# Optimization experiments

Measured on AMD Instinct MI355X. Metric: run time of the kernel, lower is better.

Reference implementation:

```python
import jax, jax.numpy as jnp
import numpy as np

B, I, H, L = 1048576, 14, 16, 8  # batch, input_size, hidden_size, num_layers


def setup_inputs() -> dict:
    key = jax.random.key(0)
    ks = jax.random.split(key, 9)
    s = 1.0 / np.sqrt(H)  # torch LSTM init scale
    return {
        "x": jax.random.normal(ks[0], (B, I), dtype=jnp.float32),
        "W_ih0": jax.random.uniform(ks[1], (4 * H, I), minval=-s, maxval=s),
        "W_ih": jax.random.uniform(ks[2], (L - 1, 4 * H, H), minval=-s, maxval=s),
        "W_hh": jax.random.uniform(ks[3], (L, 4 * H, H), minval=-s, maxval=s),
        "b_ih": jax.random.uniform(ks[4], (L, 4 * H), minval=-s, maxval=s),
        "b_hh": jax.random.uniform(ks[5], (L, 4 * H), minval=-s, maxval=s),
        "fc_w": jax.random.uniform(ks[6], (1, H), minval=-s, maxval=s),
        "fc_b": jax.random.uniform(ks[7], (1,), minval=-s, maxval=s),
    }


def _cell(inp, h, c, Wi, Wh, bi, bh):
    # PyTorch gate order: i, f, g, o
    g = inp @ Wi.T + bi + h @ Wh.T + bh  # [B, 4H]
    i, f, gg, o = jnp.split(g, 4, axis=-1)
    c_new = jax.nn.sigmoid(f) * c + jax.nn.sigmoid(i) * jnp.tanh(gg)
    h_new = jax.nn.sigmoid(o) * jnp.tanh(c_new)
    return h_new, c_new


def reference(x, W_ih0, W_ih, W_hh, b_ih, b_hh, fc_w, fc_b):
    # seq_len == 1, so each nn.LSTM layer is one cell step.
    # Original quirk: for layers >= 1 the layer input AND initial hidden are
    # both the previous layer's output h; initial cell is previous layer's c.
    h = jnp.zeros((x.shape[0], H), x.dtype)
    c = jnp.zeros_like(h)
    h, c = _cell(x, h, c, W_ih0, W_hh[0], b_ih[0], b_hh[0])
    for l in range(1, L):  # fixed small layer count
        h, c = _cell(h, h, c, W_ih[l - 1], W_hh[l], b_ih[l], b_hh[l])
    return h @ fc_w.T + fc_b  # [B, 1]
```

## Files before the change

### kernel.cpp

```cpp
#include <hip/hip_runtime.h>


typedef _Float16 f16x8 __attribute__((ext_vector_type(8)));
typedef _Float16 f16x2 __attribute__((ext_vector_type(2)));
typedef float f32x4 __attribute__((ext_vector_type(4)));
typedef float f32x2 __attribute__((ext_vector_type(2)));

#if __has_builtin(__builtin_amdgcn_mfma_f32_16x16x32_f16)
__device__ __forceinline__ f32x4 mfma32h(f16x8 a, f16x8 b, f32x4 c) {
    return __builtin_amdgcn_mfma_f32_16x16x32_f16(a, b, c, 0, 0, 0);
}
#else
__device__ __forceinline__ f32x4 mfma32h(f16x8 a, f16x8 b, f32x4 c) {
    asm volatile("v_mfma_f32_16x16x32_f16 %0, %1, %2, %0\n\ts_nop 7\n\ts_nop 7"
                 : "+v"(c) : "v"(a), "v"(b));
    return c;
}
#endif

#define NLOG2E  (-1.4426950408889634f)
#define G2LOG2E (2.8853900817779268f)
#define THREADS 1024
#define WAVES_PB (THREADS / 64)
#define NBLOCKS 512
#define NTILES 3

__device__ __forceinline__ void act2(f32x2 yi, f32x2 yf, f32x2 yg, f32x2 yo,
                                     f32x2& c, f32x2& h) {
    f32x2 Ei, Ef, Eg, Eo;
    Ei[0] = __builtin_amdgcn_exp2f(yi[0]); Ei[1] = __builtin_amdgcn_exp2f(yi[1]);
    Ef[0] = __builtin_amdgcn_exp2f(yf[0]); Ef[1] = __builtin_amdgcn_exp2f(yf[1]);
    Eg[0] = __builtin_amdgcn_exp2f(yg[0]); Eg[1] = __builtin_amdgcn_exp2f(yg[1]);
    Eo[0] = __builtin_amdgcn_exp2f(yo[0]); Eo[1] = __builtin_amdgcn_exp2f(yo[1]);
    const f32x2 one = {1.f, 1.f};
    const f32x2 Di = Ei + one, Df = Ef + one, Do = Eo + one;
    const f32x2 P = __builtin_elementwise_fma(Di, Eg, Di);
    const f32x2 num = __builtin_elementwise_fma(
        Eg, Df, __builtin_elementwise_fma(c, P, -Df));
    const f32x2 DfP = Df * P;
    f32x2 R1;
    R1[0] = __builtin_amdgcn_rcpf(DfP[0]); R1[1] = __builtin_amdgcn_rcpf(DfP[1]);
    c = num * R1;
    const f32x2 cg = c * (f32x2){G2LOG2E, G2LOG2E};
    f32x2 Ec;
    Ec[0] = __builtin_amdgcn_exp2f(cg[0]); Ec[1] = __builtin_amdgcn_exp2f(cg[1]);
    const f32x2 Q = __builtin_elementwise_fma(Do, Ec, Do);
    f32x2 R2;
    R2[0] = __builtin_amdgcn_rcpf(Q[0]); R2[1] = __builtin_amdgcn_rcpf(Q[1]);
    h = __builtin_elementwise_fma(Ec, R2, -R2);
}

#define LOP(v) __builtin_shufflevector(v, v, 0, 1)
#define HIP2(v) __builtin_shufflevector(v, v, 2, 3)

__device__ __forceinline__ f16x8 make_bfrag(f32x2 ha, f32x2 hb) {
    const f16x2 p0 = __builtin_bit_cast(f16x2, __builtin_amdgcn_cvt_pkrtz(ha[0], ha[1]));
    const f16x2 p1 = __builtin_bit_cast(f16x2, __builtin_amdgcn_cvt_pkrtz(hb[0], hb[1]));
    return (f16x8){p0[0], p0[1], p1[0], p1[1], p0[0], p0[1], p1[0], p1[1]};
}

__global__ __launch_bounds__(THREADS, 2) void lstm_mfma_kernel(
    const float* __restrict__ x,
    const float* __restrict__ W_ih0,
    const float* __restrict__ W_ih,
    const float* __restrict__ W_hh,
    const float* __restrict__ b_ih,
    const float* __restrict__ b_hh,
    const float* __restrict__ fc_w,
    const float* __restrict__ fc_b,
    float* __restrict__ out,
    int nB)
{
    __shared__ __align__(16) short sWF[8 * 4 * 64 * 8];
    __shared__ __align__(16) float sB[8 * 64];
    __shared__ __align__(16) float sFC[20];

    const int tid = threadIdx.x;

    for (int slot = tid; slot < 2048; slot += THREADS) {
        const int l = slot >> 8;
        const int t = (slot >> 6) & 3;
        const int ln = slot & 63;
        const int row = t * 16 + (ln & 15);
        const int k0 = (ln >> 4) * 4;
        const float scale = (t == 2) ? G2LOG2E : NLOG2E;
        short frag[8];
        #pragma unroll
        for (int j = 0; j < 4; ++j) {
            const int k = k0 + j;
            float w;
            if (l == 0) w = (k < 14) ? W_ih0[row * 14 + k] : 0.0f;
            else        w = W_ih[(l - 1) * 1024 + row * 16 + k]
                          + W_hh[l * 1024 + row * 16 + k];
            w *= scale;
            const _Float16 wh = (_Float16)w;
            const float wres = w - (float)wh;
            const _Float16 wl = (_Float16)wres;
            frag[j]     = __builtin_bit_cast(short, wh);
            frag[4 + j] = __builtin_bit_cast(short, wl);
        }
        *(short4*)(sWF + slot * 8)     = make_short4(frag[0], frag[1], frag[2], frag[3]);
        *(short4*)(sWF + slot * 8 + 4) = make_short4(frag[4], frag[5], frag[6], frag[7]);
    }
    for (int idx = tid; idx < 512; idx += THREADS) {
        const int row = idx & 63;
        const float scale = ((row >> 4) == 2) ? G2LOG2E : NLOG2E;
        sB[idx] = (b_ih[idx] + b_hh[idx]) * scale;
    }
    if (tid < 16) sFC[tid] = fc_w[tid];
    if (tid == 16) sFC[16] = fc_b[0];
    __syncthreads();

    const int lane = tid & 63;
    const int wv = tid >> 6;
    const int bcol = lane & 15;
    const int hi = lane >> 4;

    const int n_grp = (nB + (16 * NTILES - 1)) / (16 * NTILES);
    const int waves_total = NBLOCKS * WAVES_PB;
    const int iters = (n_grp + waves_total - 1) / waves_total;
    const int gw = blockIdx.x * WAVES_PB + wv;

    const short* wbase = sWF + (lane << 3);
    const float* bbase = sB + hi * 4;

    const f32x4 fw4 = *(const f32x4*)(sFC + hi * 4);
    const f32x2 fwa = LOP(fw4), fwb = HIP2(fw4);
    const float fb = sFC[16];

    for (int it = 0; it < iters; ++it) {
        const int grp = gw * iters + it;
        if (grp >= n_grp) break;

        int bidx[NTILES];
        f32x2 ha[NTILES], hb[NTILES];
        f16x8 Bf[NTILES];
        f32x2 ca[NTILES], cb[NTILES];

        #pragma unroll
        for (int m = 0; m < NTILES; ++m) {
            const int b = grp * (16 * NTILES) + m * 16 + bcol;
            bidx[m] = b;
            const int bc = b < nB ? b : nB - 1;
            const float* xr = x + bc * 14 + hi * 4;
            const float2 p = *(const float2*)xr;
            ha[m][0] = p.x; ha[m][1] = p.y;
            if (hi < 3) {
                const float2 q = *(const float2*)(xr + 2);
                hb[m][0] = q.x; hb[m][1] = q.y;
            } else { hb[m] = (f32x2){0.f, 0.f}; }
            Bf[m] = make_bfrag(ha[m], hb[m]);
            ca[m] = (f32x2){0.f, 0.f};
            cb[m] = (f32x2){0.f, 0.f};
        }

        #pragma unroll
        for (int l = 0; l < 8; ++l) {
            f16x8 fr[4];
            f32x4 bias[4];
            #pragma unroll
            for (int t = 0; t < 4; ++t) {
                fr[t] = *(const f16x8*)(wbase + ((l * 4 + t) << 9));
                bias[t] = *(const f32x4*)(bbase + l * 64 + t * 16);
            }
            #pragma unroll
            for (int m = 0; m < NTILES; ++m) {
                f32x4 a[4];
                #pragma unroll
                for (int t = 0; t < 4; ++t) {
                    a[t] = mfma32h(fr[t], Bf[m], bias[t]);
                }
                act2(LOP(a[0]), LOP(a[1]), LOP(a[2]), LOP(a[3]), ca[m], ha[m]);
                act2(HIP2(a[0]), HIP2(a[1]), HIP2(a[2]), HIP2(a[3]), cb[m], hb[m]);
                Bf[m] = make_bfrag(ha[m], hb[m]);
            }
        }

        #pragma unroll
        for (int m = 0; m < NTILES; ++m) {
            f32x2 s = ha[m] * fwa;
            s = __builtin_elementwise_fma(hb[m], fwb, s);
            float p = s[0] + s[1];
            p += __shfl_xor(p, 16, 64);
            p += __shfl_xor(p, 32, 64);
            if (hi == 0 && bidx[m] < nB) out[bidx[m]] = p + fb;
        }
    }
}

extern "C" void kernel_launch(void* const* d_in, const int* in_sizes, int n_in,
                              void* d_out, int out_size, void* d_ws, size_t ws_size,
                              hipStream_t stream) {
    const float* x     = (const float*)d_in[0];
    const float* W_ih0 = (const float*)d_in[1];
    const float* W_ih  = (const float*)d_in[2];
    const float* W_hh  = (const float*)d_in[3];
    const float* b_ih  = (const float*)d_in[4];
    const float* b_hh  = (const float*)d_in[5];
    const float* fc_w  = (const float*)d_in[6];
    const float* fc_b  = (const float*)d_in[7];
    float* out = (float*)d_out;

    const int B = in_sizes[0] / 14;
    lstm_mfma_kernel<<<NBLOCKS, THREADS, 0, stream>>>(
        x, W_ih0, W_ih, W_hh, b_ih, b_hh, fc_w, fc_b, out, B);
}
```

Measured before the change: 124.5 us.

## Prefetch next batch group's inputs and interleave two tiles' MFMAs per layer

```diff
diff --git a/kernel.cpp b/kernel.cpp
--- a/kernel.cpp
+++ b/kernel.cpp
@@ -23,7 +23,7 @@
 #define THREADS 1024
 #define WAVES_PB (THREADS / 64)
 #define NBLOCKS 512
-#define NTILES 3
+#define NTILES 2
 
 __device__ __forceinline__ void act2(f32x2 yi, f32x2 yf, f32x2 yg, f32x2 yo,
                                      f32x2& c, f32x2& h) {
@@ -59,7 +59,7 @@
     return (f16x8){p0[0], p0[1], p1[0], p1[1], p0[0], p0[1], p1[0], p1[1]};
 }
 
-__global__ __launch_bounds__(THREADS, 2) void lstm_mfma_kernel(
+__global__ __launch_bounds__(THREADS, 8) void lstm_mfma_kernel(
     const float* __restrict__ x,
     const float* __restrict__ W_ih0,
     const float* __restrict__ W_ih,
@@ -120,6 +120,7 @@
     const int waves_total = NBLOCKS * WAVES_PB;
     const int iters = (n_grp + waves_total - 1) / waves_total;
     const int gw = blockIdx.x * WAVES_PB + wv;
+    const int grp_base = gw * iters;
 
     const short* wbase = sWF + (lane << 3);
     const float* bbase = sB + hi * 4;
@@ -128,52 +129,57 @@
     const f32x2 fwa = LOP(fw4), fwb = HIP2(fw4);
     const float fb = sFC[16];
 
+    int pf_b[NTILES];
+    float2 pf_a[NTILES], pf_q[NTILES];
+    auto prefetch = [&](int grp) {
+        #pragma unroll
+        for (int m = 0; m < NTILES; ++m) {
+            const int b = grp * (16 * NTILES) + m * 16 + bcol;
+            pf_b[m] = b;
+            const int bc = b < nB ? b : nB - 1;
+            const float* xr = x + bc * 14 + hi * 4;
+            pf_a[m] = *(const float2*)xr;
+            pf_q[m] = (hi < 3) ? *(const float2*)(xr + 2) : make_float2(0.f, 0.f);
+        }
+    };
+
+    if (grp_base < n_grp) prefetch(grp_base);
+
     for (int it = 0; it < iters; ++it) {
-        const int grp = gw * iters + it;
+        const int grp = grp_base + it;
         if (grp >= n_grp) break;
 
         int bidx[NTILES];
         f32x2 ha[NTILES], hb[NTILES];
         f16x8 Bf[NTILES];
         f32x2 ca[NTILES], cb[NTILES];
-
         #pragma unroll
         for (int m = 0; m < NTILES; ++m) {
-            const int b = grp * (16 * NTILES) + m * 16 + bcol;
-            bidx[m] = b;
-            const int bc = b < nB ? b : nB - 1;
-            const float* xr = x + bc * 14 + hi * 4;
-            const float2 p = *(const float2*)xr;
-            ha[m][0] = p.x; ha[m][1] = p.y;
-            if (hi < 3) {
-                const float2 q = *(const float2*)(xr + 2);
-                hb[m][0] = q.x; hb[m][1] = q.y;
-            } else { hb[m] = (f32x2){0.f, 0.f}; }
+            bidx[m] = pf_b[m];
+            ha[m][0] = pf_a[m].x; ha[m][1] = pf_a[m].y;
+            hb[m][0] = pf_q[m].x; hb[m][1] = pf_q[m].y;
             Bf[m] = make_bfrag(ha[m], hb[m]);
             ca[m] = (f32x2){0.f, 0.f};
             cb[m] = (f32x2){0.f, 0.f};
         }
+        if (it + 1 < iters && grp + 1 < n_grp) prefetch(grp + 1);
 
         #pragma unroll
         for (int l = 0; l < 8; ++l) {
-            f16x8 fr[4];
-            f32x4 bias[4];
+            f32x4 a0[4], a1[4];
             #pragma unroll
             for (int t = 0; t < 4; ++t) {
-                fr[t] = *(const f16x8*)(wbase + ((l * 4 + t) << 9));
-                bias[t] = *(const f32x4*)(bbase + l * 64 + t * 16);
+                const f16x8 fr = *(const f16x8*)(wbase + ((l * 4 + t) << 9));
+                const f32x4 bias = *(const f32x4*)(bbase + l * 64 + t * 16);
+                a0[t] = mfma32h(fr, Bf[0], bias);
+                a1[t] = mfma32h(fr, Bf[1], bias);
             }
-            #pragma unroll
-            for (int m = 0; m < NTILES; ++m) {
-                f32x4 a[4];
-                #pragma unroll
-                for (int t = 0; t < 4; ++t) {
-                    a[t] = mfma32h(fr[t], Bf[m], bias[t]);
-                }
-                act2(LOP(a[0]), LOP(a[1]), LOP(a[2]), LOP(a[3]), ca[m], ha[m]);
-                act2(HIP2(a[0]), HIP2(a[1]), HIP2(a[2]), HIP2(a[3]), cb[m], hb[m]);
-                Bf[m] = make_bfrag(ha[m], hb[m]);
-            }
+            act2(LOP(a0[0]), LOP(a0[1]), LOP(a0[2]), LOP(a0[3]), ca[0], ha[0]);
+            act2(HIP2(a0[0]), HIP2(a0[1]), HIP2(a0[2]), HIP2(a0[3]), cb[0], hb[0]);
+            act2(LOP(a1[0]), LOP(a1[1]), LOP(a1[2]), LOP(a1[3]), ca[1], ha[1]);
+            act2(HIP2(a1[0]), HIP2(a1[1]), HIP2(a1[2]), HIP2(a1[3]), cb[1], hb[1]);
+            Bf[0] = make_bfrag(ha[0], hb[0]);
+            Bf[1] = make_bfrag(ha[1], hb[1]);
         }
 
         #pragma unroll
```

New measurement: 115.2 us. 1.08x faster.
